# Optimization experiments

Hardware: AMD Instinct MI355X
Metric: run time of the kernel (lower is better)

## Reference

```python
import jax, jax.numpy as jnp
import numpy as np

C = 3.0e8
WAVE_LAMBDA = 0.0038
PI = float(np.pi)


def _grid(size, resolution, x_val):
    edge_left = [-i for i in range(1, size, 2)][::-1]
    edge_right = [i for i in range(1, size, 2)]
    edge = edge_left + edge_right
    if size % 2 == 1:
        edge = [i for i in range(-(size - 1), size, 2)]
    edge = np.array(edge, dtype=np.float32) * resolution / 2.0
    wx, wy = np.meshgrid(edge, edge)
    wz = np.zeros((size, size), dtype=np.float32)
    pos = np.stack((wz, wx, wy), 2).reshape(size * size, 3).astype(np.float32)
    pos[:, 0] = x_val
    return pos


def setup_inputs() -> dict:
    key = jax.random.key(0)
    k1, k2, k3 = jax.random.split(key, 3)
    lam = WAVE_LAMBDA
    f = np.arange(77e9, 81e9 + 1e9, 1e9, dtype=np.float32)  # [5]
    tx = np.array([[0, -8 * lam, 0], [0, -6 * lam, 0], [0, -4 * lam, 0], [0, -2 * lam, 0],
                   [0, 0, 0], [0, 2 * lam, 0], [0, 4 * lam, 0], [0, 6 * lam, 0], [0, 8 * lam, 0],
                   [0, -2.5 * lam, -3 * lam], [0, -3.0 * lam, -2 * lam], [0, -3.5 * lam, -0.5 * lam]],
                  dtype=np.float32)  # [12,3]
    rx = np.array([[0, -16 * lam, -0.066], [0, -15.5 * lam, -0.066], [0, -15 * lam, -0.066],
                   [0, -14.5 * lam, -0.066], [0, -10.5 * lam, -0.066], [0, -10 * lam, -0.066],
                   [0, -9.5 * lam, -0.066], [0, -9 * lam, -0.066], [0, 7 * lam, -0.066],
                   [0, 7.5 * lam, -0.066], [0, 8 * lam, -0.066], [0, 8.5 * lam, -0.066],
                   [0, 9 * lam, -0.066], [0, 9.5 * lam, -0.066], [0, 10 * lam, -0.066],
                   [0, 10.5 * lam, -0.066]], dtype=np.float32)  # [16,3]
    meta = _grid(60, 0.0015, 0.1)     # [3600,3]
    scene = _grid(20, 0.0015, 0.3)    # [400,3] (resolution reassigned to 0.0015 in torch init)
    # trainable params
    meta_theta = jax.random.uniform(k1, (3600, 1), jnp.float32,
                                    minval=-PI, maxval=20 * PI / 180.0)
    w = jax.random.normal(k2, (5, 6, 12), jnp.float32)
    T = jax.random.normal(k3, (400, 128), jnp.float32)
    return {"T": T, "w": w, "meta_theta": meta_theta, "f": jnp.asarray(f),
            "tx_positions": jnp.asarray(tx), "rx_positions": jnp.asarray(rx),
            "meta_positions": jnp.asarray(meta), "scene_positions": jnp.asarray(scene)}


def _channel(locs_start, locs_end, f):
    # pairwise distance [Ns,Ne], then complex channel [F,Ns,Ne]
    d = jnp.linalg.norm(locs_start[:, None, :] - locs_end[None, :, :], axis=2)
    return (0.001 / d ** 2) * jnp.exp(-1j * 2 * PI * f[:, None, None] * d / C)


def reference(T, w, meta_theta, f, tx_positions, rx_positions, meta_positions, scene_positions):
    theta = jnp.clip(meta_theta, -PI, 20 * PI / 180.0)[:, 0]   # [M]
    phase = jnp.exp(1j * theta)                                # [M]
    pri = jnp.exp(1j * w)                                      # [F,6,Tx]
    H1 = _channel(tx_positions, meta_positions, f)             # [F,Tx,M]
    H2 = _channel(meta_positions, scene_positions, f)          # [F,M,S]
    H3 = _channel(scene_positions, meta_positions, f)          # [F,S,M]
    H4 = _channel(meta_positions, rx_positions, f)             # [F,M,Rx]
    A = jnp.einsum('fkt,ftm->fkm', pri, H1)                    # [F,6,M]
    A = A * phase[None, None, :]
    A = jnp.einsum('fkm,fms->fks', A, H2)                      # [F,6,S]
    # diag_embed(A) @ H3  ==  per-row scaling of H3 (no dense SxS diag needed)
    A = A[..., None] * H3[:, None, :, :]                       # [F,6,S,M]
    A = A * phase[None, None, None, :]
    A = jnp.einsum('fksm,fmr->fksr', A, H4)                    # [F,6,S,Rx]
    A = jnp.transpose(A, (3, 0, 1, 2))                         # [Rx,F,6,S]
    A = jnp.tile(A, (1, 1, 12, 1))                             # [Rx,F,72,S]
    A = A.reshape(-1, A.shape[3])                              # [Rx*F*72, S]
    T_complex = T.astype(jnp.complex64)
    mic_data = A @ T_complex                                   # [Rx*F*72, B]
    s_A = jnp.concatenate([A.real, A.imag], axis=0)            # [2*Rx*F*72, S]
    s_mic = jnp.concatenate([mic_data.real, mic_data.imag], axis=0)[..., None]
    return (s_A, s_mic)
```

## Files before the change

kernel.cpp:

```cpp
#include <hip/hip_runtime.h>
#include <hip/hip_bf16.h>
#include <math.h>

#define F_N 5
#define K_N 6
#define T_N 12
#define M_N 3600
#define S_N 400
#define R_N 16
#define B_N 128

#define PI_F 3.14159265358979f
#define CLIP_HI 0.3490658503988659f
#define NEG_TWO_PI_OVER_C (-6.283185307179586f / 3.0e8f)

#define SA_BASE   0
#define MIC_BASE  4608000

#define KP 3616
#define W_ELEMS  (5 * 48 * KP)
#define H_ELEMS  (5 * 800 * KP)
#define C_ELEMS  (4 * 5 * 48 * 800)
#define WS_NEED  ((size_t)(W_ELEMS + H_ELEMS) * 2 + (size_t)C_ELEMS * 4)

typedef __attribute__((ext_vector_type(8))) short bf16x8;
typedef __attribute__((ext_vector_type(4))) float f32x4;

__device__ __forceinline__ void fast_sincos(float x, float* s, float* c) {
    float r = x * 0.15915494309189535f;
    r -= floorf(r);
    *s = __builtin_amdgcn_sinf(r);
    *c = __builtin_amdgcn_cosf(r);
}


__global__ __launch_bounds__(256) void stage_kernel(
    const float* __restrict__ w, const float* __restrict__ meta_theta,
    const float* __restrict__ fin, const float* __restrict__ txp,
    const float* __restrict__ rxp, const float* __restrict__ metap,
    const float* __restrict__ scenep,
    __hip_bfloat16* __restrict__ Wbf, __hip_bfloat16* __restrict__ Hbf)
{
    const int tid = threadIdx.x;
    const int blk = blockIdx.x;

    if (blk < 75) {
        __shared__ float pri[K_N * T_N * 2];
        __shared__ float txs[T_N * 3];
        __shared__ float rxs[R_N * 3];
        const int f = blk / 15;
        const int mblk = blk % 15;

        if (tid < K_N * T_N) {
            float sv, cv; fast_sincos(w[f * (K_N * T_N) + tid], &sv, &cv);
            pri[tid * 2] = cv; pri[tid * 2 + 1] = sv;
        }
        if (tid >= 64 && tid < 64 + T_N * 3) txs[tid - 64] = txp[tid - 64];
        if (tid >= 128 && tid < 128 + R_N * 3) rxs[tid - 128] = rxp[tid - 128];
        __syncthreads();

        const int m = mblk * 256 + tid;
        if (m >= KP) return;
        __hip_bfloat16* wb = Wbf + (size_t)f * 48 * KP + m;

        if (m >= M_N) {
            for (int row = 0; row < 48; ++row) wb[(size_t)row * KP] = __float2bfloat16(0.f);
            return;
        }

        const float px = metap[m * 3 + 0];
        const float py = metap[m * 3 + 1];
        const float pz = metap[m * 3 + 2];
        const float coef = NEG_TWO_PI_OVER_C * fin[f];

        float th = meta_theta[m];
        th = fminf(fmaxf(th, -PI_F), CLIP_HI);
        float phs, phc; fast_sincos(th, &phs, &phc);

        float hre[T_N], him[T_N];
#pragma unroll
        for (int t = 0; t < T_N; ++t) {
            float dx = txs[t * 3 + 0] - px, dy = txs[t * 3 + 1] - py, dz = txs[t * 3 + 2] - pz;
            float d = sqrtf(dx * dx + dy * dy + dz * dz);
            float amp = 1e-3f / (d * d);
            float sv, cv; fast_sincos(coef * d, &sv, &cv);
            hre[t] = amp * cv; him[t] = amp * sv;
        }
#pragma unroll
        for (int k = 0; k < K_N; ++k) {
            float ar = 0.f, ai = 0.f;
#pragma unroll
            for (int t = 0; t < T_N; ++t) {
                float pr = pri[(k * T_N + t) * 2], pim = pri[(k * T_N + t) * 2 + 1];
                ar += pr * hre[t] - pim * him[t];
                ai += pr * him[t] + pim * hre[t];
            }
            wb[(size_t)k * KP]        = __float2bfloat16(ar * phc - ai * phs);
            wb[(size_t)(22 + k) * KP] = __float2bfloat16(ar * phs + ai * phc);
        }
#pragma unroll
        for (int r = 0; r < R_N; ++r) {
            float dx = rxs[r * 3 + 0] - px, dy = rxs[r * 3 + 1] - py, dz = rxs[r * 3 + 2] - pz;
            float d = sqrtf(dx * dx + dy * dy + dz * dz);
            float amp = 1e-3f / (d * d);
            float sv, cv; fast_sincos(coef * d, &sv, &cv);
            float cr = amp * cv, ci = amp * sv;
            wb[(size_t)(6 + r) * KP]  = __float2bfloat16(cr * phc - ci * phs);
            wb[(size_t)(28 + r) * KP] = __float2bfloat16(cr * phs + ci * phc);
        }
#pragma unroll
        for (int row = 44; row < 48; ++row) wb[(size_t)row * KP] = __float2bfloat16(0.f);
    } else {
        const int q = blk - 75;
        const int f = q / S_N;
        const int s = q % S_N;
        const float coef = NEG_TWO_PI_OVER_C * fin[f];
        const float sx = scenep[s * 3 + 0];
        const float sy = scenep[s * 3 + 1];
        const float sz = scenep[s * 3 + 2];
        __hip_bfloat16* hr = Hbf + ((size_t)f * 800 + s) * KP;
        __hip_bfloat16* hi = hr + (size_t)400 * KP;

        for (int m = tid; m < KP; m += 256) {
            float re = 0.f, im = 0.f;
            if (m < M_N) {
                float px = metap[m * 3 + 0], py = metap[m * 3 + 1], pz = metap[m * 3 + 2];
                float dx = px - sx, dy = py - sy, dz = pz - sz;
                float d = sqrtf(dx * dx + dy * dy + dz * dz);
                float amp = 1e-3f / (d * d);
                float sv, cv; fast_sincos(coef * d, &sv, &cv);
                re = amp * cv; im = amp * sv;
            }
            hr[m] = __float2bfloat16(re);
            hi[m] = __float2bfloat16(im);
        }
    }
}

__global__ __launch_bounds__(128) void gemm_kernel(
    const ushort* __restrict__ Wbf, const ushort* __restrict__ Hbf,
    float* __restrict__ Cp)
{
    const int blk = blockIdx.x;
    const int f = blk / 100;
    const int rem = blk % 100;
    const int nblk = rem / 4;
    const int ksp = rem % 4;
    const int wave = threadIdx.x >> 6;
    const int lane = threadIdx.x & 63;
    const int quad = lane >> 4;
    const int l16 = lane & 15;

    const int n = nblk * 32 + wave * 16 + l16;
    const int kbeg = (ksp == 0) ? 0 : (29 + 28 * (ksp - 1));
    const int kcnt = (ksp == 0) ? 29 : 28;

    f32x4 acc0 = {0.f, 0.f, 0.f, 0.f};
    f32x4 acc1 = {0.f, 0.f, 0.f, 0.f};
    f32x4 acc2 = {0.f, 0.f, 0.f, 0.f};

    const ushort* wb = Wbf + (size_t)f * 48 * KP;
    const ushort* hrow = Hbf + ((size_t)f * 800 + n) * KP;

    for (int kk = 0; kk < kcnt; ++kk) {
        int k0 = (kbeg + kk) * 32 + quad * 8;
        bf16x8 b  = *(const bf16x8*)(hrow + k0);
        bf16x8 a0 = *(const bf16x8*)(wb + (size_t)(l16) * KP + k0);
        bf16x8 a1 = *(const bf16x8*)(wb + (size_t)(16 + l16) * KP + k0);
        bf16x8 a2 = *(const bf16x8*)(wb + (size_t)(32 + l16) * KP + k0);
        acc0 = __builtin_amdgcn_mfma_f32_16x16x32_bf16(a0, b, acc0, 0, 0, 0);
        acc1 = __builtin_amdgcn_mfma_f32_16x16x32_bf16(a1, b, acc1, 0, 0, 0);
        acc2 = __builtin_amdgcn_mfma_f32_16x16x32_bf16(a2, b, acc2, 0, 0, 0);
    }

    float* cb = Cp + ((size_t)(ksp * 5 + f) * 48) * 800;
#pragma unroll
    for (int i = 0; i < 4; ++i) {
        int row = quad * 4 + i;
        cb[(size_t)row * 800 + n]        = acc0[i];
        cb[(size_t)(16 + row) * 800 + n] = acc1[i];
        cb[(size_t)(32 + row) * 800 + n] = acc2[i];
    }
}

__device__ __forceinline__ void combineC(const float* __restrict__ Cp, int f, int row,
                                         int s, float* re, float* im) {
    float r = 0.f, i = 0.f;
#pragma unroll
    for (int p = 0; p < 4; ++p) {
        const float* c = Cp + ((size_t)(p * 5 + f) * 48) * 800;
        r += c[(size_t)row * 800 + s]       - c[(size_t)(22 + row) * 800 + 400 + s];
        i += c[(size_t)row * 800 + 400 + s] + c[(size_t)(22 + row) * 800 + s];
    }
    *re = r; *im = i;
}

#define SA_BLOCKS 750
__global__ __launch_bounds__(256) void epilogue2_kernel(
    const float* __restrict__ Cp, const float* __restrict__ T,
    float* __restrict__ out)
{
    __shared__ float cre[S_N], cim[S_N];
    __shared__ float pR[256], pI[256];
    const int tid = threadIdx.x;
    const int blk = blockIdx.x;

    if (blk < SA_BLOCKS) {
        int i = blk * 256 + tid;
        int s = i % S_N; int rest = i / S_N;
        int k = rest % K_N; rest /= K_N;
        int f = rest % F_N; int r = rest / F_N;

        float ar, ai, br, bi;
        combineC(Cp, f, k, s, &ar, &ai);
        combineC(Cp, f, 6 + r, s, &br, &bi);
        float cr = ar * br - ai * bi;
        float ci = ar * bi + ai * br;

        int base = (r * F_N + f) * 72;
#pragma unroll
        for (int j = 0; j < 12; ++j) {
            int row = base + j * K_N + k;
            out[SA_BASE + (size_t)row * S_N + s] = cr;
            out[SA_BASE + (size_t)(5760 + row) * S_N + s] = ci;
        }
    } else {
        int bk = blk - SA_BLOCKS;
        int k = bk % K_N;
        int f = (bk / K_N) % F_N;
        int r = bk / (K_N * F_N);

        for (int s = tid; s < S_N; s += 256) {
            float ar, ai, br, bi;
            combineC(Cp, f, k, s, &ar, &ai);
            combineC(Cp, f, 6 + r, s, &br, &bi);
            cre[s] = ar * br - ai * bi;
            cim[s] = ar * bi + ai * br;
        }
        __syncthreads();

        const int b = tid & 127;
        const int hs = tid >> 7;
        float accR = 0.f, accI = 0.f;
        const int sBeg = hs * 200, sEnd = sBeg + 200;
#pragma unroll 4
        for (int s = sBeg; s < sEnd; ++s) {
            float tv = T[s * B_N + b];
            accR += cre[s] * tv;
            accI += cim[s] * tv;
        }
        pR[tid] = accR; pI[tid] = accI;
        __syncthreads();
        if (tid < 128) {
            accR = pR[tid] + pR[tid + 128];
            accI = pI[tid] + pI[tid + 128];
            int base = (r * F_N + f) * 72;
#pragma unroll
            for (int j = 0; j < 12; ++j) {
                int row = base + j * K_N + k;
                out[MIC_BASE + (size_t)row * B_N + b] = accR;
                out[MIC_BASE + (size_t)(5760 + row) * B_N + b] = accI;
            }
        }
    }
}

__global__ __launch_bounds__(256) void prep_kernel(
    const float* __restrict__ w, const float* __restrict__ meta_theta,
    const float* __restrict__ fin, const float* __restrict__ txp,
    const float* __restrict__ rxp, const float* __restrict__ metap,
    float* __restrict__ A1, float* __restrict__ H4p)
{
    __shared__ float pri[K_N * T_N * 2];
    __shared__ float txs[T_N * 3];
    __shared__ float rxs[R_N * 3];
    const int tid = threadIdx.x;
    const int f = blockIdx.x / 15;
    const int mblk = blockIdx.x % 15;

    if (tid < K_N * T_N) {
        float sv, cv; fast_sincos(w[f * (K_N * T_N) + tid], &sv, &cv);
        pri[tid * 2] = cv; pri[tid * 2 + 1] = sv;
    }
    if (tid >= 64 && tid < 64 + T_N * 3) txs[tid - 64] = txp[tid - 64];
    if (tid >= 128 && tid < 128 + R_N * 3) rxs[tid - 128] = rxp[tid - 128];
    __syncthreads();

    const int m = mblk * 256 + tid;
    if (m >= M_N) return;

    const float px = metap[m * 3 + 0];
    const float py = metap[m * 3 + 1];
    const float pz = metap[m * 3 + 2];
    const float coef = NEG_TWO_PI_OVER_C * fin[f];

    float th = meta_theta[m];
    th = fminf(fmaxf(th, -PI_F), CLIP_HI);
    float phs, phc; fast_sincos(th, &phs, &phc);

    float hre[T_N], him[T_N];
#pragma unroll
    for (int t = 0; t < T_N; ++t) {
        float dx = txs[t * 3 + 0] - px, dy = txs[t * 3 + 1] - py, dz = txs[t * 3 + 2] - pz;
        float d = sqrtf(dx * dx + dy * dy + dz * dz);
        float amp = 1e-3f / (d * d);
        float sv, cv; fast_sincos(coef * d, &sv, &cv);
        hre[t] = amp * cv; him[t] = amp * sv;
    }
    float* a1 = A1 + ((size_t)f * M_N + m) * (K_N * 2);
#pragma unroll
    for (int k = 0; k < K_N; ++k) {
        float ar = 0.f, ai = 0.f;
#pragma unroll
        for (int t = 0; t < T_N; ++t) {
            float pr = pri[(k * T_N + t) * 2], pim = pri[(k * T_N + t) * 2 + 1];
            ar += pr * hre[t] - pim * him[t];
            ai += pr * him[t] + pim * hre[t];
        }
        a1[k * 2]     = ar * phc - ai * phs;
        a1[k * 2 + 1] = ar * phs + ai * phc;
    }
    float* h4 = H4p + ((size_t)f * M_N + m) * (R_N * 2);
#pragma unroll
    for (int r = 0; r < R_N; ++r) {
        float dx = rxs[r * 3 + 0] - px, dy = rxs[r * 3 + 1] - py, dz = rxs[r * 3 + 2] - pz;
        float d = sqrtf(dx * dx + dy * dy + dz * dz);
        float amp = 1e-3f / (d * d);
        float sv, cv; fast_sincos(coef * d, &sv, &cv);
        float cr = amp * cv, ci = amp * sv;
        h4[r * 2]     = cr * phc - ci * phs;
        h4[r * 2 + 1] = cr * phs + ci * phc;
    }
}

__global__ __launch_bounds__(256, 2) void main_kernel(
    const float* __restrict__ fin, const float* __restrict__ metap,
    const float* __restrict__ scenep, const float* __restrict__ A1,
    const float* __restrict__ H4p, float* __restrict__ A2, float* __restrict__ Bm)
{
    const int f = blockIdx.x / 200;
    const int sq = blockIdx.x % 200;
    const int s0 = 2 * sq, s1 = s0 + 1;
    const int tid = threadIdx.x;

    const float coef = NEG_TWO_PI_OVER_C * fin[f];
    const float sx0 = scenep[s0 * 3], sy0 = scenep[s0 * 3 + 1], sz0 = scenep[s0 * 3 + 2];
    const float sx1 = scenep[s1 * 3], sy1 = scenep[s1 * 3 + 1], sz1 = scenep[s1 * 3 + 2];

    float acc[88];
#pragma unroll
    for (int i = 0; i < 88; ++i) acc[i] = 0.f;

    const float4* a1base = (const float4*)(A1 + (size_t)f * M_N * (K_N * 2));
    const float4* h4base = (const float4*)(H4p + (size_t)f * M_N * (R_N * 2));

    for (int m = tid; m < M_N; m += 256) {
        float px = metap[m * 3 + 0], py = metap[m * 3 + 1], pz = metap[m * 3 + 2];
        float dx0 = px - sx0, dy0 = py - sy0, dz0 = pz - sz0;
        float d0 = sqrtf(dx0 * dx0 + dy0 * dy0 + dz0 * dz0);
        float dx1 = px - sx1, dy1 = py - sy1, dz1 = pz - sz1;
        float d1 = sqrtf(dx1 * dx1 + dy1 * dy1 + dz1 * dz1);
        float sv0, cv0, sv1, cv1;
        fast_sincos(coef * d0, &sv0, &cv0);
        fast_sincos(coef * d1, &sv1, &cv1);
        float amp0 = 1e-3f / (d0 * d0), amp1 = 1e-3f / (d1 * d1);
        float h2r0 = amp0 * cv0, h2i0 = amp0 * sv0;
        float h2r1 = amp1 * cv1, h2i1 = amp1 * sv1;

        const float4* a1 = a1base + (size_t)m * 3;
#pragma unroll
        for (int q = 0; q < 3; ++q) {
            float4 v = a1[q];
            acc[4 * q + 0] += v.x * h2r0 - v.y * h2i0;
            acc[4 * q + 1] += v.x * h2i0 + v.y * h2r0;
            acc[4 * q + 2] += v.z * h2r0 - v.w * h2i0;
            acc[4 * q + 3] += v.z * h2i0 + v.w * h2r0;
            acc[44 + 4 * q + 0] += v.x * h2r1 - v.y * h2i1;
            acc[44 + 4 * q + 1] += v.x * h2i1 + v.y * h2r1;
            acc[44 + 4 * q + 2] += v.z * h2r1 - v.w * h2i1;
            acc[44 + 4 * q + 3] += v.z * h2i1 + v.w * h2r1;
        }
        const float4* h4 = h4base + (size_t)m * 8;
#pragma unroll
        for (int q = 0; q < 8; ++q) {
            float4 v = h4[q];
            acc[12 + 4 * q + 0] += v.x * h2r0 - v.y * h2i0;
            acc[12 + 4 * q + 1] += v.x * h2i0 + v.y * h2r0;
            acc[12 + 4 * q + 2] += v.z * h2r0 - v.w * h2i0;
            acc[12 + 4 * q + 3] += v.z * h2i0 + v.w * h2r0;
            acc[56 + 4 * q + 0] += v.x * h2r1 - v.y * h2i1;
            acc[56 + 4 * q + 1] += v.x * h2i1 + v.y * h2r1;
            acc[56 + 4 * q + 2] += v.z * h2r1 - v.w * h2i1;
            acc[56 + 4 * q + 3] += v.z * h2i1 + v.w * h2r1;
        }
    }

#pragma unroll
    for (int off = 32; off > 0; off >>= 1) {
#pragma unroll
        for (int i = 0; i < 88; ++i) acc[i] += __shfl_down(acc[i], off);
    }
    __shared__ float red[4][88];
    const int wave = tid >> 6, lane = tid & 63;
    if (lane == 0) {
#pragma unroll
        for (int i = 0; i < 88; ++i) red[wave][i] = acc[i];
    }
    __syncthreads();
    if (tid < 88) {
        float v = red[0][tid] + red[1][tid] + red[2][tid] + red[3][tid];
        int half = tid / 44, slot = tid - 44 * half;
        int s = half ? s1 : s0;
        if (slot < 12) {
            int k = slot >> 1, c = slot & 1;
            A2[(((size_t)f * K_N + k) * S_N + s) * 2 + c] = v;
        } else {
            int j = slot - 12; int r = j >> 1, c = j & 1;
            Bm[(((size_t)f * S_N + s) * R_N + r) * 2 + c] = v;
        }
    }
}

__global__ __launch_bounds__(256) void epilogue_kernel(
    const float* __restrict__ A2, const float* __restrict__ Bm,
    const float* __restrict__ T, float* __restrict__ out)
{
    __shared__ float cre[S_N], cim[S_N];
    __shared__ float pR[256], pI[256];
    const int tid = threadIdx.x;
    const int blk = blockIdx.x;

    if (blk < SA_BLOCKS) {
        int i = blk * 256 + tid;
        int s = i % S_N; int rest = i / S_N;
        int k = rest % K_N; rest /= K_N;
        int f = rest % F_N; int r = rest / F_N;

        float ar = A2[((f * K_N + k) * S_N + s) * 2];
        float ai = A2[((f * K_N + k) * S_N + s) * 2 + 1];
        float br = Bm[((f * S_N + s) * R_N + r) * 2];
        float bi = Bm[((f * S_N + s) * R_N + r) * 2 + 1];
        float cr = ar * br - ai * bi;
        float ci = ar * bi + ai * br;

        int base = (r * F_N + f) * 72;
#pragma unroll
        for (int j = 0; j < 12; ++j) {
            int row = base + j * K_N + k;
            out[SA_BASE + (size_t)row * S_N + s] = cr;
            out[SA_BASE + (size_t)(5760 + row) * S_N + s] = ci;
        }
    } else {
        int bk = blk - SA_BLOCKS;
        int k = bk % K_N;
        int f = (bk / K_N) % F_N;
        int r = bk / (K_N * F_N);

        for (int s = tid; s < S_N; s += 256) {
            float ar = A2[((f * K_N + k) * S_N + s) * 2];
            float ai = A2[((f * K_N + k) * S_N + s) * 2 + 1];
            float br = Bm[((f * S_N + s) * R_N + r) * 2];
            float bi = Bm[((f * S_N + s) * R_N + r) * 2 + 1];
            cre[s] = ar * br - ai * bi;
            cim[s] = ar * bi + ai * br;
        }
        __syncthreads();

        const int b = tid & 127;
        const int hs = tid >> 7;
        float accR = 0.f, accI = 0.f;
        const int sBeg = hs * 200, sEnd = sBeg + 200;
#pragma unroll 4
        for (int s = sBeg; s < sEnd; ++s) {
            float tv = T[s * B_N + b];
            accR += cre[s] * tv;
            accI += cim[s] * tv;
        }
        pR[tid] = accR; pI[tid] = accI;
        __syncthreads();
        if (tid < 128) {
            accR = pR[tid] + pR[tid + 128];
            accI = pI[tid] + pI[tid + 128];
            int base = (r * F_N + f) * 72;
#pragma unroll
            for (int j = 0; j < 12; ++j) {
                int row = base + j * K_N + k;
                out[MIC_BASE + (size_t)row * B_N + b] = accR;
                out[MIC_BASE + (size_t)(5760 + row) * B_N + b] = accI;
            }
        }
    }
}

extern "C" void kernel_launch(void* const* d_in, const int* in_sizes, int n_in,
                              void* d_out, int out_size, void* d_ws, size_t ws_size,
                              hipStream_t stream) {
    const float* T  = (const float*)d_in[0];
    const float* w  = (const float*)d_in[1];
    const float* th = (const float*)d_in[2];
    const float* fr = (const float*)d_in[3];
    const float* tx = (const float*)d_in[4];
    const float* rx = (const float*)d_in[5];
    const float* mp = (const float*)d_in[6];
    const float* sp = (const float*)d_in[7];

    float* out = (float*)d_out;

    if (ws_size >= WS_NEED) {
        __hip_bfloat16* Wbf = (__hip_bfloat16*)d_ws;
        __hip_bfloat16* Hbf = Wbf + W_ELEMS;
        float* Cp = (float*)(Hbf + H_ELEMS);

        stage_kernel<<<75 + 2000, 256, 0, stream>>>(w, th, fr, tx, rx, mp, sp, Wbf, Hbf);
        gemm_kernel<<<500, 128, 0, stream>>>((const ushort*)Wbf, (const ushort*)Hbf, Cp);
        epilogue2_kernel<<<SA_BLOCKS + 480, 256, 0, stream>>>(Cp, T, out);
    } else {
        float* ws  = (float*)d_ws;
        float* A1  = ws;
        float* H4p = ws + 216000;
        float* A2  = ws + 792000;
        float* Bm  = ws + 816000;

        prep_kernel<<<75, 256, 0, stream>>>(w, th, fr, tx, rx, mp, A1, H4p);
        main_kernel<<<F_N * 200, 256, 0, stream>>>(fr, mp, sp, A1, H4p, A2, Bm);
        epilogue_kernel<<<SA_BLOCKS + 480, 256, 0, stream>>>(A2, Bm, T, out);
    }
}
```

Before: 124.0 us.

## Store W and H bf16 operands in k-block-major tiled layout for contiguous MFMA loads

Reorganizes the bf16 W and H workspace buffers from row-major with a long K stride into 32-wide K-blocks, each holding all rows contiguously. Each GEMM k-step then reads a contiguous chunk instead of rows strided by KP, which should improve coalescing and cache locality of the MFMA operand loads. The producer stage now writes in the tiled layout, so its stores are scattered in 32-element pieces rather than running along a full row.

```diff
diff --git a/kernel.cpp b/kernel.cpp
--- a/kernel.cpp
+++ b/kernel.cpp
@@ -17,7 +17,8 @@
 #define SA_BASE   0
 #define MIC_BASE  4608000
 
-#define KP 3616
+#define NK 113
+#define KP (NK * 32)
 #define W_ELEMS  (5 * 48 * KP)
 #define H_ELEMS  (5 * 800 * KP)
 #define C_ELEMS  (4 * 5 * 48 * 800)
@@ -61,10 +62,10 @@
 
         const int m = mblk * 256 + tid;
         if (m >= KP) return;
-        __hip_bfloat16* wb = Wbf + (size_t)f * 48 * KP + m;
+        __hip_bfloat16* wb = Wbf + ((size_t)(f * NK + (m >> 5)) * 48) * 32 + (m & 31);
 
         if (m >= M_N) {
-            for (int row = 0; row < 48; ++row) wb[(size_t)row * KP] = __float2bfloat16(0.f);
+            for (int row = 0; row < 48; ++row) wb[row * 32] = __float2bfloat16(0.f);
             return;
         }
 
@@ -95,8 +96,8 @@
                 ar += pr * hre[t] - pim * him[t];
                 ai += pr * him[t] + pim * hre[t];
             }
-            wb[(size_t)k * KP]        = __float2bfloat16(ar * phc - ai * phs);
-            wb[(size_t)(22 + k) * KP] = __float2bfloat16(ar * phs + ai * phc);
+            wb[k * 32]        = __float2bfloat16(ar * phc - ai * phs);
+            wb[(22 + k) * 32] = __float2bfloat16(ar * phs + ai * phc);
         }
 #pragma unroll
         for (int r = 0; r < R_N; ++r) {
@@ -105,11 +106,11 @@
             float amp = 1e-3f / (d * d);
             float sv, cv; fast_sincos(coef * d, &sv, &cv);
             float cr = amp * cv, ci = amp * sv;
-            wb[(size_t)(6 + r) * KP]  = __float2bfloat16(cr * phc - ci * phs);
-            wb[(size_t)(28 + r) * KP] = __float2bfloat16(cr * phs + ci * phc);
-        }
-#pragma unroll
-        for (int row = 44; row < 48; ++row) wb[(size_t)row * KP] = __float2bfloat16(0.f);
+            wb[(6 + r) * 32]  = __float2bfloat16(cr * phc - ci * phs);
+            wb[(28 + r) * 32] = __float2bfloat16(cr * phs + ci * phc);
+        }
+#pragma unroll
+        for (int row = 44; row < 48; ++row) wb[row * 32] = __float2bfloat16(0.f);
     } else {
         const int q = blk - 75;
         const int f = q / S_N;
@@ -118,8 +119,6 @@
         const float sx = scenep[s * 3 + 0];
         const float sy = scenep[s * 3 + 1];
         const float sz = scenep[s * 3 + 2];
-        __hip_bfloat16* hr = Hbf + ((size_t)f * 800 + s) * KP;
-        __hip_bfloat16* hi = hr + (size_t)400 * KP;
 
         for (int m = tid; m < KP; m += 256) {
             float re = 0.f, im = 0.f;
@@ -131,8 +130,9 @@
                 float sv, cv; fast_sincos(coef * d, &sv, &cv);
                 re = amp * cv; im = amp * sv;
             }
-            hr[m] = __float2bfloat16(re);
-            hi[m] = __float2bfloat16(im);
+            size_t idx = ((size_t)(f * NK + (m >> 5)) * 800 + s) * 32 + (m & 31);
+            Hbf[idx] = __float2bfloat16(re);
+            Hbf[idx + 400 * 32] = __float2bfloat16(im);
         }
     }
 }
@@ -159,15 +159,13 @@
     f32x4 acc1 = {0.f, 0.f, 0.f, 0.f};
     f32x4 acc2 = {0.f, 0.f, 0.f, 0.f};
 
-    const ushort* wb = Wbf + (size_t)f * 48 * KP;
-    const ushort* hrow = Hbf + ((size_t)f * 800 + n) * KP;
-
     for (int kk = 0; kk < kcnt; ++kk) {
-        int k0 = (kbeg + kk) * 32 + quad * 8;
-        bf16x8 b  = *(const bf16x8*)(hrow + k0);
-        bf16x8 a0 = *(const bf16x8*)(wb + (size_t)(l16) * KP + k0);
-        bf16x8 a1 = *(const bf16x8*)(wb + (size_t)(16 + l16) * KP + k0);
-        bf16x8 a2 = *(const bf16x8*)(wb + (size_t)(32 + l16) * KP + k0);
+        const int kb = kbeg + kk;
+        bf16x8 b  = *(const bf16x8*)(Hbf + ((size_t)(f * NK + kb) * 800 + n) * 32 + quad * 8);
+        const ushort* wbase = Wbf + ((size_t)(f * NK + kb) * 48) * 32 + quad * 8;
+        bf16x8 a0 = *(const bf16x8*)(wbase + (size_t)l16 * 32);
+        bf16x8 a1 = *(const bf16x8*)(wbase + (size_t)(16 + l16) * 32);
+        bf16x8 a2 = *(const bf16x8*)(wbase + (size_t)(32 + l16) * 32);
         acc0 = __builtin_amdgcn_mfma_f32_16x16x32_bf16(a0, b, acc0, 0, 0, 0);
         acc1 = __builtin_amdgcn_mfma_f32_16x16x32_bf16(a1, b, acc1, 0, 0, 0);
         acc2 = __builtin_amdgcn_mfma_f32_16x16x32_bf16(a2, b, acc2, 0, 0, 0);
```

Measured after the change: 122.8 us. About the same (-1.0%).
